# Kernel optimization log

Hardware: AMD Instinct MI355X
Metric: run time of the kernel (lower is better)

Reference implementation:

```python
import jax, jax.numpy as jnp
import numpy as np

N_NODES = 50000
N_EDGES = 600000
D_IN = 128
D_OUT = 128
K_HOPS = 3


def setup_inputs() -> dict:
    key = jax.random.key(0)
    k1, k2, k3 = jax.random.split(key, 3)
    V = jnp.arange(N_NODES, dtype=jnp.int64)
    E = jax.random.randint(k1, (2, N_EDGES), 0, N_NODES, dtype=jnp.int64)
    X = jax.random.normal(k2, (N_NODES, D_IN), dtype=jnp.float32)
    W = jax.random.normal(k3, (D_OUT, D_IN), dtype=jnp.float32) * (1.0 / np.sqrt(D_IN))
    b = jnp.zeros((D_OUT,), dtype=jnp.float32)
    return {"V": V, "E": E, "X": X, "W": W, "b": b}


def reference(V, E, X, W, b):
    # SGConv: H = (D^-1/2 (A + I) D^-1/2)^K X, then Linear(H)
    N = X.shape[0]
    self_loop = jnp.arange(N, dtype=E.dtype)
    src = jnp.concatenate([E[0], self_loop])  # [n_edges + N]
    dst = jnp.concatenate([E[1], self_loop])
    ones = jnp.ones(src.shape[0], dtype=X.dtype)
    deg = jax.ops.segment_sum(ones, dst, num_segments=N)  # includes self loops
    dinv = jnp.where(deg > 0, jax.lax.rsqrt(deg), 0.0)
    norm = dinv[src] * dinv[dst]  # [n_edges + N]
    H = X
    for _ in range(K_HOPS):
        msgs = norm[:, None] * H[src]  # gather + scale
        H = jax.ops.segment_sum(msgs, dst, num_segments=N)  # scatter-add
    return H @ W.T + b
```

## Files before the change

### kernel.cpp

```cpp
#include <hip/hip_runtime.h>

#define DIM 128


__global__ void k_count(const int* __restrict__ dst, int* __restrict__ cnt, int ne) {
    int i = blockIdx.x * blockDim.x + threadIdx.x;
    if (i < ne) atomicAdd(&cnt[dst[i]], 1);
}

__global__ void k_dinv(const int* __restrict__ cnt, float* __restrict__ dinv, int n) {
    int i = blockIdx.x * blockDim.x + threadIdx.x;
    if (i < n) dinv[i] = rsqrtf((float)cnt[i] + 1.0f);
}

__global__ __launch_bounds__(1024) void k_scan(const int* __restrict__ cnt,
                                               int* __restrict__ rowptr, int n) {
    __shared__ int sums[1024];
    int t = threadIdx.x;
    int chunk = (n + 1023) >> 10;
    int lo = t * chunk, hi = min(lo + chunk, n);
    int s = 0;
    for (int i = lo; i < hi; ++i) s += cnt[i];
    sums[t] = s;
    __syncthreads();
    for (int off = 1; off < 1024; off <<= 1) {
        int v = (t >= off) ? sums[t - off] : 0;
        __syncthreads();
        if (t >= off) sums[t] += v;
        __syncthreads();
    }
    int run = (t > 0) ? sums[t - 1] : 0;
    for (int i = lo; i < hi; ++i) { rowptr[i] = run; run += cnt[i]; }
    if (t == 0) rowptr[n] = sums[1023];
}

__global__ void k_bin(const int* __restrict__ src, const int* __restrict__ dst,
                      int* __restrict__ cnt, const int* __restrict__ rowptr,
                      int* __restrict__ col, int ne) {
    int e = blockIdx.x * blockDim.x + threadIdx.x;
    if (e >= ne) return;
    int t = dst[e];
    int pos = rowptr[t] + atomicSub(&cnt[t], 1) - 1;
    col[pos] = src[e];
}

__global__ void k_prescale(const float* __restrict__ X, const float* __restrict__ dinv,
                           float* __restrict__ Hs, int n) {
    int i = blockIdx.x * blockDim.x + threadIdx.x;
    int total = n * (DIM / 4);
    if (i >= total) return;
    int node = i >> 5;
    float w = dinv[node];
    float4 v = ((const float4*)X)[i];
    v.x *= w; v.y *= w; v.z *= w; v.w *= w;
    ((float4*)Hs)[i] = v;
}


__global__ __launch_bounds__(256) void k_pull(const int* __restrict__ rowptr,
                                              const int* __restrict__ col,
                                              const float* __restrict__ dinv,
                                              const float* __restrict__ Hc,
                                              float* __restrict__ Hn, int n, int last) {
    int wid = (blockIdx.x * blockDim.x + threadIdx.x) >> 6;
    if (wid >= n) return;
    int lane = threadIdx.x & 63;
    const float2* __restrict__ base = (const float2*)Hc;
    size_t li = (size_t)wid * 64 + lane;

    float2 acc = base[li];
    int e0 = rowptr[wid], e1 = rowptr[wid + 1];
    int e = e0;
    for (; e + 3 < e1; e += 4) {
        int s0 = col[e], s1 = col[e + 1], s2 = col[e + 2], s3 = col[e + 3];
        float2 a = base[(size_t)s0 * 64 + lane];
        float2 b = base[(size_t)s1 * 64 + lane];
        float2 c = base[(size_t)s2 * 64 + lane];
        float2 d = base[(size_t)s3 * 64 + lane];
        acc.x += (a.x + b.x) + (c.x + d.x);
        acc.y += (a.y + b.y) + (c.y + d.y);
    }
    for (; e < e1; ++e) {
        int s = col[e];
        float2 a = base[(size_t)s * 64 + lane];
        acc.x += a.x;
        acc.y += a.y;
    }
    float w = dinv[wid];
    float scale = last ? w : w * w;
    acc.x *= scale; acc.y *= scale;
    ((float2*)Hn)[li] = acc;
}


__global__ __launch_bounds__(256) void k_gemm(const float* __restrict__ H,
                                              const float* __restrict__ W,
                                              const float* __restrict__ b,
                                              float* __restrict__ out, int n) {
    __shared__ float Wt[DIM * DIM];
    int tid = threadIdx.x;
    for (int idx = tid; idx < DIM * DIM; idx += 256) {
        int d = idx >> 7;
        int j = idx & (DIM - 1);
        Wt[d * DIM + j] = W[j * DIM + d];
    }
    __syncthreads();

    int lane = tid & 63;
    int wv   = tid >> 6;
    int j0   = lane * 2;
    int row0 = blockIdx.x * 32 + wv * 8;

    float2 bias = make_float2(b[j0], b[j0 + 1]);
    float2 acc[8];
    const float* hp[8];
    #pragma unroll
    for (int r = 0; r < 8; ++r) {
        acc[r] = bias;
        int rc = row0 + r; if (rc > n - 1) rc = n - 1;
        hp[r] = H + (size_t)rc * DIM;
    }

    for (int d4 = 0; d4 < DIM / 4; ++d4) {
        float4 hv[8];
        #pragma unroll
        for (int r = 0; r < 8; ++r) hv[r] = *(const float4*)(hp[r] + d4 * 4);
        float2 w0 = *(const float2*)&Wt[(d4 * 4 + 0) * DIM + j0];
        float2 w1 = *(const float2*)&Wt[(d4 * 4 + 1) * DIM + j0];
        float2 w2 = *(const float2*)&Wt[(d4 * 4 + 2) * DIM + j0];
        float2 w3 = *(const float2*)&Wt[(d4 * 4 + 3) * DIM + j0];
        #pragma unroll
        for (int r = 0; r < 8; ++r) {
            acc[r].x = fmaf(hv[r].x, w0.x, acc[r].x);
            acc[r].y = fmaf(hv[r].x, w0.y, acc[r].y);
            acc[r].x = fmaf(hv[r].y, w1.x, acc[r].x);
            acc[r].y = fmaf(hv[r].y, w1.y, acc[r].y);
            acc[r].x = fmaf(hv[r].z, w2.x, acc[r].x);
            acc[r].y = fmaf(hv[r].z, w2.y, acc[r].y);
            acc[r].x = fmaf(hv[r].w, w3.x, acc[r].x);
            acc[r].y = fmaf(hv[r].w, w3.y, acc[r].y);
        }
    }

    #pragma unroll
    for (int r = 0; r < 8; ++r) {
        int row = row0 + r;
        if (row < n) *(float2*)(out + (size_t)row * DIM + j0) = acc[r];
    }
}


extern "C" void kernel_launch(void* const* d_in, const int* in_sizes, int n_in,
                              void* d_out, int out_size, void* d_ws, size_t ws_size,
                              hipStream_t stream) {
    const int*   E = (const int*)d_in[1];
    const float* X = (const float*)d_in[2];
    const float* W = (const float*)d_in[3];
    const float* b = (const float*)d_in[4];

    int n  = in_sizes[0];
    int ne = in_sizes[1] / 2;
    const int* src = E;
    const int* dst = E + ne;

    char* ws = (char*)d_ws;
    float* dinv   = (float*)(ws + 0);
    int*   cnt    = (int*)  (ws + 262144);
    int*   rowptr = (int*)  (ws + 524288);
    int*   col    = (int*)  (ws + 786432);
    float* Hws    = (float*)(ws + 3211264);
    float* Hout   = (float*)d_out;

    const int T = 256;
    int gN  = (n + T - 1) / T;
    int gE  = (ne + T - 1) / T;
    int gNV = (n * (DIM / 4) + T - 1) / T;
    int gW  = (n * 64 + T - 1) / T;

    hipMemsetAsync(cnt, 0, (size_t)n * 4, stream);
    k_count<<<gE, T, 0, stream>>>(dst, cnt, ne);
    k_dinv<<<gN, T, 0, stream>>>(cnt, dinv, n);
    k_scan<<<1, 1024, 0, stream>>>(cnt, rowptr, n);
    k_bin<<<gE, T, 0, stream>>>(src, dst, cnt, rowptr, col, ne);

    k_prescale<<<gNV, T, 0, stream>>>(X, dinv, Hout, n);
    k_pull<<<gW, T, 0, stream>>>(rowptr, col, dinv, Hout, Hws,  n, 0);
    k_pull<<<gW, T, 0, stream>>>(rowptr, col, dinv, Hws,  Hout, n, 0);
    k_pull<<<gW, T, 0, stream>>>(rowptr, col, dinv, Hout, Hws,  n, 1);

    k_gemm<<<(n + 31) / 32, 256, 0, stream>>>(Hws, W, b, Hout, n);
}
```

Before: 396.1 us.

## Use half-wave float4 gathers in SpMM and split GEMM output columns across blocks

The pull kernel now assigns 32 lanes per node with float4 loads instead of 64 lanes with float2. Each wave handles two destination nodes, which halves the wave count and widens each gather access. The GEMM kernel splits the 128 output columns across two blocks, loads only half of W into padded shared memory without a transpose, and software-prefetches the next H chunk. It also cuts rows per thread to 4, lowering register pressure and shared memory per block at the cost of reading H twice.

```diff
diff --git a/kernel.cpp b/kernel.cpp
--- a/kernel.cpp
+++ b/kernel.cpp
@@ -62,34 +62,35 @@
                                               const float* __restrict__ dinv,
                                               const float* __restrict__ Hc,
                                               float* __restrict__ Hn, int n, int last) {
-    int wid = (blockIdx.x * blockDim.x + threadIdx.x) >> 6;
-    if (wid >= n) return;
-    int lane = threadIdx.x & 63;
-    const float2* __restrict__ base = (const float2*)Hc;
-    size_t li = (size_t)wid * 64 + lane;
-
-    float2 acc = base[li];
-    int e0 = rowptr[wid], e1 = rowptr[wid + 1];
+    int hw = (blockIdx.x * blockDim.x + threadIdx.x) >> 5;
+    if (hw >= n) return;
+    int lane = threadIdx.x & 31;
+    const float4* __restrict__ base = (const float4*)Hc;
+    size_t li = (size_t)hw * 32 + lane;
+
+    float4 acc = base[li];
+    int e0 = rowptr[hw], e1 = rowptr[hw + 1];
     int e = e0;
-    for (; e + 3 < e1; e += 4) {
+    for (; e + 4 <= e1; e += 4) {
         int s0 = col[e], s1 = col[e + 1], s2 = col[e + 2], s3 = col[e + 3];
-        float2 a = base[(size_t)s0 * 64 + lane];
-        float2 b = base[(size_t)s1 * 64 + lane];
-        float2 c = base[(size_t)s2 * 64 + lane];
-        float2 d = base[(size_t)s3 * 64 + lane];
+        float4 a = base[(size_t)s0 * 32 + lane];
+        float4 b = base[(size_t)s1 * 32 + lane];
+        float4 c = base[(size_t)s2 * 32 + lane];
+        float4 d = base[(size_t)s3 * 32 + lane];
         acc.x += (a.x + b.x) + (c.x + d.x);
         acc.y += (a.y + b.y) + (c.y + d.y);
+        acc.z += (a.z + b.z) + (c.z + d.z);
+        acc.w += (a.w + b.w) + (c.w + d.w);
     }
     for (; e < e1; ++e) {
         int s = col[e];
-        float2 a = base[(size_t)s * 64 + lane];
-        acc.x += a.x;
-        acc.y += a.y;
-    }
-    float w = dinv[wid];
-    float scale = last ? w : w * w;
-    acc.x *= scale; acc.y *= scale;
-    ((float2*)Hn)[li] = acc;
+        float4 a = base[(size_t)s * 32 + lane];
+        acc.x += a.x; acc.y += a.y; acc.z += a.z; acc.w += a.w;
+    }
+    float w = dinv[hw];
+    float sc = last ? w : w * w;
+    acc.x *= sc; acc.y *= sc; acc.z *= sc; acc.w *= sc;
+    ((float4*)Hn)[li] = acc;
 }
 
 
@@ -97,53 +98,66 @@
                                               const float* __restrict__ W,
                                               const float* __restrict__ b,
                                               float* __restrict__ out, int n) {
-    __shared__ float Wt[DIM * DIM];
+    __shared__ float Wt[64][DIM + 1];
     int tid = threadIdx.x;
-    for (int idx = tid; idx < DIM * DIM; idx += 256) {
-        int d = idx >> 7;
-        int j = idx & (DIM - 1);
-        Wt[d * DIM + j] = W[j * DIM + d];
+    int jb  = blockIdx.x & 1;
+    int rb  = blockIdx.x >> 1;
+
+    const float4* Wv = (const float4*)(W + (size_t)jb * 64 * DIM);
+    for (int idx = tid; idx < 64 * 32; idx += 256) {
+        int jj = idx >> 5;
+        int dq = idx & 31;
+        float4 v = Wv[idx];
+        *(float4*)&Wt[jj][dq * 4] = v;
     }
     __syncthreads();
 
     int lane = tid & 63;
     int wv   = tid >> 6;
-    int j0   = lane * 2;
-    int row0 = blockIdx.x * 32 + wv * 8;
+    int cp   = lane & 31;
+    int rg   = lane >> 5;
+    int j0   = jb * 64 + cp * 2;
+    int row0 = rb * 32 + wv * 8 + rg * 4;
 
     float2 bias = make_float2(b[j0], b[j0 + 1]);
-    float2 acc[8];
-    const float* hp[8];
+    float2 acc[4];
+    const float* hp[4];
     #pragma unroll
-    for (int r = 0; r < 8; ++r) {
+    for (int r = 0; r < 4; ++r) {
         acc[r] = bias;
         int rc = row0 + r; if (rc > n - 1) rc = n - 1;
         hp[r] = H + (size_t)rc * DIM;
     }
 
+    float4 cur[4];
+    #pragma unroll
+    for (int r = 0; r < 4; ++r) cur[r] = *(const float4*)(hp[r]);
+
     for (int d4 = 0; d4 < DIM / 4; ++d4) {
-        float4 hv[8];
+        float4 nxt[4];
+        if (d4 + 1 < DIM / 4) {
+            #pragma unroll
+            for (int r = 0; r < 4; ++r) nxt[r] = *(const float4*)(hp[r] + (d4 + 1) * 4);
+        }
+        float4 wa = *(const float4*)&Wt[cp * 2 + 0][d4 * 4];
+        float4 wb = *(const float4*)&Wt[cp * 2 + 1][d4 * 4];
         #pragma unroll
-        for (int r = 0; r < 8; ++r) hv[r] = *(const float4*)(hp[r] + d4 * 4);
-        float2 w0 = *(const float2*)&Wt[(d4 * 4 + 0) * DIM + j0];
-        float2 w1 = *(const float2*)&Wt[(d4 * 4 + 1) * DIM + j0];
-        float2 w2 = *(const float2*)&Wt[(d4 * 4 + 2) * DIM + j0];
-        float2 w3 = *(const float2*)&Wt[(d4 * 4 + 3) * DIM + j0];
+        for (int r = 0; r < 4; ++r) {
+            acc[r].x = fmaf(cur[r].x, wa.x, acc[r].x);
+            acc[r].y = fmaf(cur[r].x, wb.x, acc[r].y);
+            acc[r].x = fmaf(cur[r].y, wa.y, acc[r].x);
+            acc[r].y = fmaf(cur[r].y, wb.y, acc[r].y);
+            acc[r].x = fmaf(cur[r].z, wa.z, acc[r].x);
+            acc[r].y = fmaf(cur[r].z, wb.z, acc[r].y);
+            acc[r].x = fmaf(cur[r].w, wa.w, acc[r].x);
+            acc[r].y = fmaf(cur[r].w, wb.w, acc[r].y);
+        }
         #pragma unroll
-        for (int r = 0; r < 8; ++r) {
-            acc[r].x = fmaf(hv[r].x, w0.x, acc[r].x);
-            acc[r].y = fmaf(hv[r].x, w0.y, acc[r].y);
-            acc[r].x = fmaf(hv[r].y, w1.x, acc[r].x);
-            acc[r].y = fmaf(hv[r].y, w1.y, acc[r].y);
-            acc[r].x = fmaf(hv[r].z, w2.x, acc[r].x);
-            acc[r].y = fmaf(hv[r].z, w2.y, acc[r].y);
-            acc[r].x = fmaf(hv[r].w, w3.x, acc[r].x);
-            acc[r].y = fmaf(hv[r].w, w3.y, acc[r].y);
-        }
+        for (int r = 0; r < 4; ++r) cur[r] = nxt[r];
     }
 
     #pragma unroll
-    for (int r = 0; r < 8; ++r) {
+    for (int r = 0; r < 4; ++r) {
         int row = row0 + r;
         if (row < n) *(float2*)(out + (size_t)row * DIM + j0) = acc[r];
     }
@@ -175,7 +189,7 @@
     int gN  = (n + T - 1) / T;
     int gE  = (ne + T - 1) / T;
     int gNV = (n * (DIM / 4) + T - 1) / T;
-    int gW  = (n * 64 + T - 1) / T;
+    int gHW = (n * 32 + T - 1) / T;
 
     hipMemsetAsync(cnt, 0, (size_t)n * 4, stream);
     k_count<<<gE, T, 0, stream>>>(dst, cnt, ne);
@@ -184,9 +198,9 @@
     k_bin<<<gE, T, 0, stream>>>(src, dst, cnt, rowptr, col, ne);
 
     k_prescale<<<gNV, T, 0, stream>>>(X, dinv, Hout, n);
-    k_pull<<<gW, T, 0, stream>>>(rowptr, col, dinv, Hout, Hws,  n, 0);
-    k_pull<<<gW, T, 0, stream>>>(rowptr, col, dinv, Hws,  Hout, n, 0);
-    k_pull<<<gW, T, 0, stream>>>(rowptr, col, dinv, Hout, Hws,  n, 1);
-
-    k_gemm<<<(n + 31) / 32, 256, 0, stream>>>(Hws, W, b, Hout, n);
-}
+    k_pull<<<gHW, T, 0, stream>>>(rowptr, col, dinv, Hout, Hws,  n, 0);
+    k_pull<<<gHW, T, 0, stream>>>(rowptr, col, dinv, Hws,  Hout, n, 0);
+    k_pull<<<gHW, T, 0, stream>>>(rowptr, col, dinv, Hout, Hws,  n, 1);
+
+    k_gemm<<<((n + 31) / 32) * 2, 256, 0, stream>>>(Hws, W, b, Hout, n);
+}
```

New measurement: 346.5 us. -12.5%, faster.
